# Kernel tuning notes

Hardware: AMD Instinct MI355X
Metric: run time of the kernel (lower is better)

Reference implementation:

```python
import jax, jax.numpy as jnp
import numpy as np

D_MODEL = 1024
EXPAND = 2
D_INNER = D_MODEL * EXPAND  # 2048
D_CONV = 4
B, T = 4, 4096
LN_EPS = 1e-5


def setup_inputs() -> dict:
    key = jax.random.key(0)
    ks = jax.random.split(key, 6)
    x = jax.random.normal(ks[0], (B, T, D_MODEL), dtype=jnp.float32)
    gamma = jnp.ones((D_MODEL,), jnp.float32)
    beta = jnp.zeros((D_MODEL,), jnp.float32)
    # in_proj: Linear(d_model -> 2*d_inner, bias=False); torch weight [out,in]
    W_in = jax.random.normal(ks[1], (2 * D_INNER, D_MODEL), jnp.float32) / np.sqrt(D_MODEL)
    # depthwise conv1d: weight [d_inner, 1, d_conv], bias [d_inner]
    conv_w = jax.random.normal(ks[2], (D_INNER, 1, D_CONV), jnp.float32) / np.sqrt(D_CONV)
    conv_b = jax.random.normal(ks[3], (D_INNER,), jnp.float32) * 0.01
    # out_proj: Linear(d_inner -> d_model, bias=False)
    W_out = jax.random.normal(ks[4], (D_MODEL, D_INNER), jnp.float32) / np.sqrt(D_INNER)
    return {"x": x, "gamma": gamma, "beta": beta, "W_in": W_in,
            "conv_w": conv_w, "conv_b": conv_b, "W_out": W_out}


def _silu(v):
    return v * jax.nn.sigmoid(v)


def reference(x, gamma, beta, W_in, conv_w, conv_b, W_out):
    residual = x
    # LayerNorm
    mu = jnp.mean(x, axis=-1, keepdims=True)
    var = jnp.mean(jnp.square(x - mu), axis=-1, keepdims=True)
    xn = (x - mu) * jax.lax.rsqrt(var + LN_EPS) * gamma + beta
    # in_proj -> split gate
    xz = jnp.einsum('btd,ed->bte', xn, W_in)  # [B,T,2*D_INNER]
    x_part, z = jnp.split(xz, 2, axis=-1)
    # causal depthwise conv: torch pads both sides by d_conv-1 then slices [:T]
    # == left pad (d_conv-1), no right pad
    lhs = jnp.transpose(x_part, (0, 2, 1))  # [B, D_INNER, T]
    x_conv = jax.lax.conv_general_dilated(
        lhs, conv_w, window_strides=(1,), padding=[(D_CONV - 1, 0)],
        feature_group_count=D_INNER,
        dimension_numbers=('NCH', 'OIH', 'NCH')) + conv_b[None, :, None]
    x_conv = jnp.transpose(x_conv, (0, 2, 1))  # [B,T,D_INNER]
    y = _silu(x_conv) * _silu(z)
    out = jnp.einsum('bte,de->btd', y, W_out)
    return residual + out  # dropout=0 (eval) -> identity
```

## Files before the change

kernel.cpp:

```cpp
#include <hip/hip_runtime.h>
#include <hip/hip_bf16.h>

#define D_MODEL 1024
#define D_INNER 2048
#define NTOK    16384
#define TLEN    4096
#define LN_EPS  1e-5f

typedef unsigned short u16;
typedef unsigned short u16x4 __attribute__((ext_vector_type(4)));
typedef unsigned short u16x8 __attribute__((ext_vector_type(8)));
typedef __bf16        bf16x8 __attribute__((ext_vector_type(8)));
typedef float         f32x4  __attribute__((ext_vector_type(4)));

__device__ __forceinline__ float b2f(u16 u) {
    union { float f; unsigned int i; } v; v.i = ((unsigned int)u) << 16; return v.f;
}
__device__ __forceinline__ u16 f2b(float f) {
    union { float f; unsigned int i; } v; v.f = f;
    unsigned int r = v.i + 0x7fffu + ((v.i >> 16) & 1u);
    return (u16)(r >> 16);
}

__device__ __forceinline__ void gld_lds16(const u16* g, u16* l) {
    __builtin_amdgcn_global_load_lds(
        (const __attribute__((address_space(1))) void*)g,
        (__attribute__((address_space(3))) void*)l, 16, 0, 0);
}

__device__ __forceinline__ void ln_body(
    int row, int tid,
    const float* __restrict__ x, const float* __restrict__ gamma,
    const float* __restrict__ beta, u16* __restrict__ xn)
{
    const float* xr = x + (size_t)row * D_MODEL;
    const int c0 = tid * 4;

    f32x4 xv = *(const f32x4*)(xr + c0);
    float s = 0.f, s2 = 0.f;
#pragma unroll
    for (int i = 0; i < 4; i++) { s += xv[i]; s2 += xv[i] * xv[i]; }

#pragma unroll
    for (int off = 32; off > 0; off >>= 1) {
        s  += __shfl_down(s,  off);
        s2 += __shfl_down(s2, off);
    }
    __shared__ float red[8];
    const int wave = tid >> 6, lane = tid & 63;
    if (lane == 0) { red[wave] = s; red[4 + wave] = s2; }
    __syncthreads();
    const float ts  = red[0] + red[1] + red[2] + red[3];
    const float ts2 = red[4] + red[5] + red[6] + red[7];
    const float mu  = ts * (1.0f / D_MODEL);
    const float var = ts2 * (1.0f / D_MODEL) - mu * mu;
    const float inv = rsqrtf(var + LN_EPS);

    f32x4 gv = *(const f32x4*)(gamma + c0);
    f32x4 bv = *(const f32x4*)(beta + c0);
    u16x4 out;
#pragma unroll
    for (int i = 0; i < 4; i++)
        out[i] = f2b((xv[i] - mu) * inv * gv[i] + bv[i]);
    *(u16x4*)(xn + (size_t)row * D_MODEL + c0) = out;
}

__global__ __launch_bounds__(256) void prep_kernel(
    const float* __restrict__ x, const float* __restrict__ gamma,
    const float* __restrict__ beta, u16* __restrict__ xn,
    const float* __restrict__ W_in, u16* __restrict__ wbin,
    const float* __restrict__ W_out, u16* __restrict__ wbout,
    const float* __restrict__ conv_w, float* __restrict__ wt,
    int lnRows)
{
    const int b   = blockIdx.x;
    const int tid = threadIdx.x;

    if (b < lnRows) {
        ln_body(b, tid, x, gamma, beta, xn);
        return;
    }
    int rb = b - lnRows;
    if (rb < 4096) {
        const int o = (rb * 256 + tid) * 4;
        f32x4 v = *(const f32x4*)(W_in + o);
        u16x4 w;
#pragma unroll
        for (int j = 0; j < 4; j++) w[j] = f2b(v[j]);
        *(u16x4*)(wbin + o) = w;
        return;
    }
    rb -= 4096;
    if (rb < 2048) {
        const int o = (rb * 256 + tid) * 4;
        f32x4 v = *(const f32x4*)(W_out + o);
        u16x4 w;
#pragma unroll
        for (int j = 0; j < 4; j++) w[j] = f2b(v[j]);
        *(u16x4*)(wbout + o) = w;
        return;
    }
    rb -= 2048;
    const int i = rb * 256 + tid;
    const int ch = i >> 2, j = i & 3;
    wt[j * D_INNER + ch] = conv_w[i];
}

__global__ __launch_bounds__(256) void ln_kernel(
    const float* __restrict__ x, const float* __restrict__ gamma,
    const float* __restrict__ beta, u16* __restrict__ xn)
{
    ln_body(blockIdx.x, threadIdx.x, x, gamma, beta, xn);
}

#define BAR()      __builtin_amdgcn_s_barrier()
#define WAIT_VM8() asm volatile("s_waitcnt vmcnt(8)" ::: "memory")
#define WAIT_VM4() asm volatile("s_waitcnt vmcnt(4)" ::: "memory")
#define WAIT_VM0() asm volatile("s_waitcnt vmcnt(0)" ::: "memory")

#define STAGE_A(ldsb, s0, s1, kt) do { \
    gld_lds16(Ag + (size_t)(s0) * K + (kt) + goff, &(ldsb)[(s0) * 64]); \
    gld_lds16(Ag + (size_t)(s1) * K + (kt) + goff, &(ldsb)[(s1) * 64]); \
} while (0)
#define STAGE_B(ldsb, s0, s1, kt) do { \
    gld_lds16(Bg + (size_t)(s0) * K + (kt) + goff, &(ldsb)[(s0) * 64]); \
    gld_lds16(Bg + (size_t)(s1) * K + (kt) + goff, &(ldsb)[(s1) * 64]); \
} while (0)

#define RD_A(base, roff) do { \
    _Pragma("unroll") for (int m_ = 0; m_ < 4; m_++) { \
        const u16* p_ = (base) + (arow0 + (roff) + m_ * 16) * 64; \
        aF[m_][0] = __builtin_bit_cast(bf16x8, *(const u16x8*)(p_ + cx0)); \
        aF[m_][1] = __builtin_bit_cast(bf16x8, *(const u16x8*)(p_ + cx1)); \
    } } while (0)
#define RD_B(base, dst, roff) do { \
    _Pragma("unroll") for (int n_ = 0; n_ < 2; n_++) { \
        const u16* p_ = (base) + (brow0 + (roff) + n_ * 16) * 64; \
        dst[n_][0] = __builtin_bit_cast(bf16x8, *(const u16x8*)(p_ + cx0)); \
        dst[n_][1] = __builtin_bit_cast(bf16x8, *(const u16x8*)(p_ + cx1)); \
    } } while (0)

#define MMA_Q(m0, n0, BB) do { \
    __builtin_amdgcn_s_setprio(1); \
    _Pragma("unroll") for (int m_ = 0; m_ < 4; m_++) \
    _Pragma("unroll") for (int n_ = 0; n_ < 2; n_++) \
    _Pragma("unroll") for (int k_ = 0; k_ < 2; k_++) \
        acc[(m0) + m_][(n0) + n_] = __builtin_amdgcn_mfma_f32_16x16x32_bf16( \
            aF[m_][k_], BB[n_][k_], acc[(m0) + m_][(n0) + n_], 0, 0, 0); \
    __builtin_amdgcn_s_setprio(0); \
} while (0)

template<bool OUT_F32>
__global__ __launch_bounds__(512, 2) void gemm256(
    const u16* __restrict__ A, const u16* __restrict__ Bt,
    void* __restrict__ Cv, const float* __restrict__ Res,
    int M, int N, int K)
{
    __shared__ u16 As[2][256 * 64];
    __shared__ u16 Bs[2][256 * 64];

    const int tid  = threadIdx.x;
    const int wave = tid >> 6;
    const int lane = tid & 63;
    const int wm = wave >> 2, wn = wave & 3;
    const int lane15 = lane & 15, quad = lane >> 4;

    const int gx   = gridDim.x;
    const int nwg  = gx * gridDim.y;
    const int flat = blockIdx.y * gx + blockIdx.x;
    const int q8   = nwg >> 3;
    const int swz  = (flat & 7) * q8 + (flat >> 3);
    const int bm = swz % gx, bn = swz / gx;

    const u16* Ag = A  + (size_t)bm * 256 * K;
    const u16* Bg = Bt + (size_t)bn * 256 * K;

    const int lrow = lane >> 3;
    const int lcol = ((lane & 7) ^ lrow) * 8;
    const size_t goff = (size_t)lrow * K + lcol;

    const int aEv0 = wave * 8,      aEv1 = 128 + wave * 8;
    const int aOd0 = 64 + wave * 8, aOd1 = 192 + wave * 8;
    const int bEv0 = (wave >> 2) * 64 + (wave & 3) * 8, bEv1 = 128 + bEv0;
    const int bOd0 = bEv0 + 32,     bOd1 = bEv1 + 32;

    const int arow0 = wm * 128 + lane15;
    const int brow0 = wn * 64  + lane15;
    const int sw8   = lane15 & 7;
    const int cx0   = ((quad ^ sw8) << 3);
    const int cx1   = cx0 ^ 32;

    f32x4  acc[8][4] = {};
    bf16x8 aF[4][2], bX[2][2], bY[2][2];

    const int NT = K >> 6;
    const int NI = NT >> 1;

    STAGE_A(As[0], aEv0, aEv1, 0);
    STAGE_B(Bs[0], bEv0, bEv1, 0);
    STAGE_A(As[0], aOd0, aOd1, 0);
    STAGE_B(Bs[0], bOd0, bOd1, 0);
    STAGE_A(As[1], aEv0, aEv1, 64);
    STAGE_B(Bs[1], bEv0, bEv1, 64);
    STAGE_A(As[1], aOd0, aOd1, 64);
    STAGE_B(Bs[1], bOd0, bOd1, 64);
    WAIT_VM0();
    BAR();
    RD_A(As[0], 0);
    RD_B(Bs[0], bX, 0);

    for (int i = 0; i < NI; i++) {
        const bool more = (i + 1 < NI);
#pragma unroll
        for (int h = 0; h < 2; h++) {
            u16* as  = As[h];
            u16* bs  = Bs[h];
            const u16* asn = As[h ^ 1];
            const u16* bsn = Bs[h ^ 1];
            const int ktS  = i * 128 + 128 + h * 64;
            const bool gN  = (h == 0) || more;
            const bool gS  = more;
            const bool lastT = (h == 1) && !more;

            if (lastT) WAIT_VM0(); else WAIT_VM8();
            BAR();
            RD_B(bs, bY, 32);
            MMA_Q(0, 0, bX);

            BAR();
            MMA_Q(0, 2, bY);
            RD_A(as, 64);

            if (!lastT) WAIT_VM4();
            BAR();
            MMA_Q(4, 0, bX);
            if (gN) RD_B(bsn, bX, 0);
            if (gS) { STAGE_A(as, aEv0, aEv1, ktS); STAGE_B(bs, bEv0, bEv1, ktS); }

            BAR();
            MMA_Q(4, 2, bY);
            if (gN) RD_A(asn, 0);
            if (gS) { STAGE_A(as, aOd0, aOd1, ktS); STAGE_B(bs, bOd0, bOd1, ktS); }
        }
    }

    const int m0 = bm * 256 + wm * 128 + quad * 4;
    const int n0 = bn * 256 + wn * 64 + lane15;
#pragma unroll
    for (int mf = 0; mf < 8; mf++) {
#pragma unroll
        for (int nf = 0; nf < 4; nf++) {
#pragma unroll
            for (int i = 0; i < 4; i++) {
                const int r  = m0 + mf * 16 + i;
                const int cc = n0 + nf * 16;
                const size_t idx = (size_t)r * N + cc;
                float v = acc[mf][nf][i];
                if (OUT_F32) {
                    ((float*)Cv)[idx] = v + Res[idx];
                } else {
                    ((u16*)Cv)[idx] = f2b(v);
                }
            }
        }
    }
}

__global__ __launch_bounds__(256) void conv_gate8(
    const u16* __restrict__ xz, const float* __restrict__ wt,
    const float* __restrict__ conv_b, u16* __restrict__ y)
{
    const int tid  = threadIdx.x;
    const int row0 = blockIdx.x * 8;
    const int c    = tid * 8;
    const int t0   = row0 & (TLEN - 1);

    float w[4][8];
#pragma unroll
    for (int j = 0; j < 4; j++) {
        f32x4 a = *(const f32x4*)(wt + j * D_INNER + c);
        f32x4 b = *(const f32x4*)(wt + j * D_INNER + c + 4);
#pragma unroll
        for (int u = 0; u < 4; u++) { w[j][u] = a[u]; w[j][4 + u] = b[u]; }
    }
    float bias[8];
    {
        f32x4 a = *(const f32x4*)(conv_b + c);
        f32x4 b = *(const f32x4*)(conv_b + c + 4);
#pragma unroll
        for (int u = 0; u < 4; u++) { bias[u] = a[u]; bias[4 + u] = b[u]; }
    }

    u16x8 xv[11];
    if (t0 != 0) {
#pragma unroll
        for (int k = 0; k < 3; k++)
            xv[k] = *(const u16x8*)(xz + (size_t)(row0 - 3 + k) * 4096 + c);
    } else {
#pragma unroll
        for (int k = 0; k < 3; k++) xv[k] = (u16x8)0;
    }
#pragma unroll
    for (int k = 3; k < 11; k++)
        xv[k] = *(const u16x8*)(xz + (size_t)(row0 - 3 + k) * 4096 + c);

#pragma unroll
    for (int i = 0; i < 8; i++) {
        float acc[8];
#pragma unroll
        for (int u = 0; u < 8; u++) acc[u] = bias[u];
#pragma unroll
        for (int j = 0; j < 4; j++)
#pragma unroll
            for (int u = 0; u < 8; u++)
                acc[u] += b2f(xv[i + j][u]) * w[j][u];

        u16x8 zv = *(const u16x8*)(xz + (size_t)(row0 + i) * 4096 + 2048 + c);
        u16x8 out;
#pragma unroll
        for (int u = 0; u < 8; u++) {
            const float a = acc[u];
            const float z = b2f(zv[u]);
            const float sa = a / (1.0f + __expf(-a));
            const float sz = z / (1.0f + __expf(-z));
            out[u] = f2b(sa * sz);
        }
        *(u16x8*)(y + (size_t)(row0 + i) * (size_t)D_INNER + c) = out;
    }
}

extern "C" void kernel_launch(void* const* d_in, const int* in_sizes, int n_in,
                              void* d_out, int out_size, void* d_ws, size_t ws_size,
                              hipStream_t stream)
{
    const float* x      = (const float*)d_in[0];
    const float* gamma  = (const float*)d_in[1];
    const float* beta   = (const float*)d_in[2];
    const float* W_in   = (const float*)d_in[3];
    const float* conv_w = (const float*)d_in[4];
    const float* conv_b = (const float*)d_in[5];
    const float* W_out  = (const float*)d_in[6];
    float* out = (float*)d_out;

    const int nWin  = 4096 * 1024;
    const int nWout = 1024 * 2048;
    const int nWc   = D_INNER * 4;

    u16*   wbin  = (u16*)d_ws;
    u16*   wbout = wbin + nWin;
    float* wt    = (float*)(wbout + nWout);
    u16*   base  = (u16*)(wt + nWc);

    const size_t wbytes = (size_t)(nWin + nWout) * sizeof(u16) + nWc * sizeof(float);
    const size_t perRow = (size_t)(D_MODEL + 4096 + D_INNER) * sizeof(u16);
    int NC = 4;
    if (ws_size >= wbytes + (size_t)NTOK * perRow)          NC = 1;
    else if (ws_size >= wbytes + (size_t)(NTOK/2) * perRow) NC = 2;
    const int RC = NTOK / NC;

    u16* xn = base;
    u16* xz = xn + (size_t)RC * D_MODEL;
    u16* y  = xz + (size_t)RC * 4096;

    const int lnRows = (NC == 1) ? NTOK : 0;
    prep_kernel<<<lnRows + 4096 + 2048 + 32, 256, 0, stream>>>(
        x, gamma, beta, xn, W_in, wbin, W_out, wbout, conv_w, wt, lnRows);

    for (int c = 0; c < NC; c++) {
        const float* xc   = x   + (size_t)c * RC * D_MODEL;
        float*       outc = out + (size_t)c * RC * D_MODEL;

        if (NC > 1)
            ln_kernel<<<RC, 256, 0, stream>>>(xc, gamma, beta, xn);

        dim3 g1(RC / 256, (2 * D_INNER) / 256);
        gemm256<false><<<g1, 512, 0, stream>>>(xn, wbin, xz, nullptr,
                                               RC, 2 * D_INNER, D_MODEL);

        conv_gate8<<<RC / 8, 256, 0, stream>>>(xz, wt, conv_b, y);

        dim3 g2(RC / 256, D_MODEL / 256);
        gemm256<true><<<g2, 512, 0, stream>>>(y, wbout, outc, xc,
                                              RC, D_MODEL, D_INNER);
    }
}
```

Measured before the change: 389.6 us.

## Restructure GEMM to 4 waves with 128x128 per-wave tiles

The 256x256 GEMM block goes from 8 waves (512 threads, 2 blocks/CU) to 4 waves (256 threads, 1 block/CU). Each wave now computes a 128x128 sub-tile with 8x8 accumulators, and staging loads are redistributed so each wave issues four loads per stage. The MFMA setprio hints are removed and the vmcnt waits are adjusted for the larger per-wave load count. This raises per-wave reuse of LDS fragments and cuts LDS read traffic, but it lowers occupancy and greatly increases register pressure (256 accumulator floats per lane), which risks spills and less latency hiding.

```diff
diff --git a/kernel.cpp b/kernel.cpp
--- a/kernel.cpp
+++ b/kernel.cpp
@@ -113,45 +113,35 @@
     ln_body(blockIdx.x, threadIdx.x, x, gamma, beta, xn);
 }
 
-#define BAR()      __builtin_amdgcn_s_barrier()
-#define WAIT_VM8() asm volatile("s_waitcnt vmcnt(8)" ::: "memory")
-#define WAIT_VM4() asm volatile("s_waitcnt vmcnt(4)" ::: "memory")
-#define WAIT_VM0() asm volatile("s_waitcnt vmcnt(0)" ::: "memory")
-
-#define STAGE_A(ldsb, s0, s1, kt) do { \
-    gld_lds16(Ag + (size_t)(s0) * K + (kt) + goff, &(ldsb)[(s0) * 64]); \
-    gld_lds16(Ag + (size_t)(s1) * K + (kt) + goff, &(ldsb)[(s1) * 64]); \
+#define BAR()       __builtin_amdgcn_s_barrier()
+#define WAIT_VM16() asm volatile("s_waitcnt vmcnt(16)" ::: "memory")
+#define WAIT_VM8()  asm volatile("s_waitcnt vmcnt(8)" ::: "memory")
+#define WAIT_VM0()  asm volatile("s_waitcnt vmcnt(0)" ::: "memory")
+
+#define STAGE4(gp, ldsb, c0, kt) do { \
+    gld_lds16((gp) + (size_t)(c0)         * K + (kt) + goff, &(ldsb)[(c0)         * 64]); \
+    gld_lds16((gp) + (size_t)((c0) +   8) * K + (kt) + goff, &(ldsb)[((c0) +   8) * 64]); \
+    gld_lds16((gp) + (size_t)((c0) + 128) * K + (kt) + goff, &(ldsb)[((c0) + 128) * 64]); \
+    gld_lds16((gp) + (size_t)((c0) + 136) * K + (kt) + goff, &(ldsb)[((c0) + 136) * 64]); \
 } while (0)
-#define STAGE_B(ldsb, s0, s1, kt) do { \
-    gld_lds16(Bg + (size_t)(s0) * K + (kt) + goff, &(ldsb)[(s0) * 64]); \
-    gld_lds16(Bg + (size_t)(s1) * K + (kt) + goff, &(ldsb)[(s1) * 64]); \
-} while (0)
-
-#define RD_A(base, roff) do { \
-    _Pragma("unroll") for (int m_ = 0; m_ < 4; m_++) { \
-        const u16* p_ = (base) + (arow0 + (roff) + m_ * 16) * 64; \
-        aF[m_][0] = __builtin_bit_cast(bf16x8, *(const u16x8*)(p_ + cx0)); \
-        aF[m_][1] = __builtin_bit_cast(bf16x8, *(const u16x8*)(p_ + cx1)); \
+
+#define RD4(dst, base, row0, roff) do { \
+    _Pragma("unroll") for (int t_ = 0; t_ < 4; t_++) { \
+        const u16* p_ = (base) + ((row0) + (roff) + t_ * 16) * 64; \
+        dst[t_][0] = __builtin_bit_cast(bf16x8, *(const u16x8*)(p_ + cx0)); \
+        dst[t_][1] = __builtin_bit_cast(bf16x8, *(const u16x8*)(p_ + cx1)); \
     } } while (0)
-#define RD_B(base, dst, roff) do { \
-    _Pragma("unroll") for (int n_ = 0; n_ < 2; n_++) { \
-        const u16* p_ = (base) + (brow0 + (roff) + n_ * 16) * 64; \
-        dst[n_][0] = __builtin_bit_cast(bf16x8, *(const u16x8*)(p_ + cx0)); \
-        dst[n_][1] = __builtin_bit_cast(bf16x8, *(const u16x8*)(p_ + cx1)); \
-    } } while (0)
-
-#define MMA_Q(m0, n0, BB) do { \
-    __builtin_amdgcn_s_setprio(1); \
+
+#define MMA_Q(m0, n0, AA, BB) do { \
     _Pragma("unroll") for (int m_ = 0; m_ < 4; m_++) \
-    _Pragma("unroll") for (int n_ = 0; n_ < 2; n_++) \
+    _Pragma("unroll") for (int n_ = 0; n_ < 4; n_++) \
     _Pragma("unroll") for (int k_ = 0; k_ < 2; k_++) \
         acc[(m0) + m_][(n0) + n_] = __builtin_amdgcn_mfma_f32_16x16x32_bf16( \
-            aF[m_][k_], BB[n_][k_], acc[(m0) + m_][(n0) + n_], 0, 0, 0); \
-    __builtin_amdgcn_s_setprio(0); \
+            AA[m_][k_], BB[n_][k_], acc[(m0) + m_][(n0) + n_], 0, 0, 0); \
 } while (0)
 
 template<bool OUT_F32>
-__global__ __launch_bounds__(512, 2) void gemm256(
+__global__ __launch_bounds__(256, 1) void gemm256(
     const u16* __restrict__ A, const u16* __restrict__ Bt,
     void* __restrict__ Cv, const float* __restrict__ Res,
     int M, int N, int K)
@@ -162,7 +152,7 @@
     const int tid  = threadIdx.x;
     const int wave = tid >> 6;
     const int lane = tid & 63;
-    const int wm = wave >> 2, wn = wave & 3;
+    const int wm2 = wave >> 1, wn2 = wave & 1;
     const int lane15 = lane & 15, quad = lane >> 4;
 
     const int gx   = gridDim.x;
@@ -179,42 +169,36 @@
     const int lcol = ((lane & 7) ^ lrow) * 8;
     const size_t goff = (size_t)lrow * K + lcol;
 
-    const int aEv0 = wave * 8,      aEv1 = 128 + wave * 8;
-    const int aOd0 = 64 + wave * 8, aOd1 = 192 + wave * 8;
-    const int bEv0 = (wave >> 2) * 64 + (wave & 3) * 8, bEv1 = 128 + bEv0;
-    const int bOd0 = bEv0 + 32,     bOd1 = bEv1 + 32;
-
-    const int arow0 = wm * 128 + lane15;
-    const int brow0 = wn * 64  + lane15;
+    const int sEv = wave * 16;
+    const int sOd = 64 + wave * 16;
+
+    const int arow0 = wm2 * 128 + lane15;
+    const int brow0 = wn2 * 128 + lane15;
     const int sw8   = lane15 & 7;
     const int cx0   = ((quad ^ sw8) << 3);
     const int cx1   = cx0 ^ 32;
 
-    f32x4  acc[8][4] = {};
-    bf16x8 aF[4][2], bX[2][2], bY[2][2];
+    f32x4  acc[8][8] = {};
+    bf16x8 a0[4][2], a1[4][2], b0[4][2], b1[4][2];
 
     const int NT = K >> 6;
     const int NI = NT >> 1;
 
-    STAGE_A(As[0], aEv0, aEv1, 0);
-    STAGE_B(Bs[0], bEv0, bEv1, 0);
-    STAGE_A(As[0], aOd0, aOd1, 0);
-    STAGE_B(Bs[0], bOd0, bOd1, 0);
-    STAGE_A(As[1], aEv0, aEv1, 64);
-    STAGE_B(Bs[1], bEv0, bEv1, 64);
-    STAGE_A(As[1], aOd0, aOd1, 64);
-    STAGE_B(Bs[1], bOd0, bOd1, 64);
-    WAIT_VM0();
+    STAGE4(Ag, As[0], sEv, 0);  STAGE4(Bg, Bs[0], sEv, 0);
+    STAGE4(Ag, As[0], sOd, 0);  STAGE4(Bg, Bs[0], sOd, 0);
+    STAGE4(Ag, As[1], sEv, 64); STAGE4(Bg, Bs[1], sEv, 64);
+    STAGE4(Ag, As[1], sOd, 64); STAGE4(Bg, Bs[1], sOd, 64);
+    WAIT_VM16();
     BAR();
-    RD_A(As[0], 0);
-    RD_B(Bs[0], bX, 0);
+    RD4(a0, As[0], arow0, 0);
+    RD4(b0, Bs[0], brow0, 0);
 
     for (int i = 0; i < NI; i++) {
         const bool more = (i + 1 < NI);
 #pragma unroll
         for (int h = 0; h < 2; h++) {
-            u16* as  = As[h];
-            u16* bs  = Bs[h];
+            u16* as = As[h];
+            u16* bs = Bs[h];
             const u16* asn = As[h ^ 1];
             const u16* bsn = Bs[h ^ 1];
             const int ktS  = i * 128 + 128 + h * 64;
@@ -222,34 +206,33 @@
             const bool gS  = more;
             const bool lastT = (h == 1) && !more;
 
-            if (lastT) WAIT_VM0(); else WAIT_VM8();
+            if (lastT) WAIT_VM0(); else WAIT_VM16();
             BAR();
-            RD_B(bs, bY, 32);
-            MMA_Q(0, 0, bX);
+            RD4(b1, bs, brow0, 64);
+            MMA_Q(0, 0, a0, b0);
 
             BAR();
-            MMA_Q(0, 2, bY);
-            RD_A(as, 64);
-
-            if (!lastT) WAIT_VM4();
+            MMA_Q(0, 4, a0, b1);
+            RD4(a1, as, arow0, 64);
+
+            if (!lastT) WAIT_VM8();
             BAR();
-            MMA_Q(4, 0, bX);
-            if (gN) RD_B(bsn, bX, 0);
-            if (gS) { STAGE_A(as, aEv0, aEv1, ktS); STAGE_B(bs, bEv0, bEv1, ktS); }
+            MMA_Q(4, 0, a1, b0);
+            if (gS) { STAGE4(Ag, as, sEv, ktS); STAGE4(Bg, bs, sEv, ktS); }
 
             BAR();
-            MMA_Q(4, 2, bY);
-            if (gN) RD_A(asn, 0);
-            if (gS) { STAGE_A(as, aOd0, aOd1, ktS); STAGE_B(bs, bOd0, bOd1, ktS); }
+            MMA_Q(4, 4, a1, b1);
+            if (gN) { RD4(b0, bsn, brow0, 0); RD4(a0, asn, arow0, 0); }
+            if (gS) { STAGE4(Ag, as, sOd, ktS); STAGE4(Bg, bs, sOd, ktS); }
         }
     }
 
-    const int m0 = bm * 256 + wm * 128 + quad * 4;
-    const int n0 = bn * 256 + wn * 64 + lane15;
+    const int m0 = bm * 256 + wm2 * 128 + quad * 4;
+    const int n0 = bn * 256 + wn2 * 128 + lane15;
 #pragma unroll
     for (int mf = 0; mf < 8; mf++) {
 #pragma unroll
-        for (int nf = 0; nf < 4; nf++) {
+        for (int nf = 0; nf < 8; nf++) {
 #pragma unroll
             for (int i = 0; i < 4; i++) {
                 const int r  = m0 + mf * 16 + i;
@@ -374,13 +357,13 @@
             ln_kernel<<<RC, 256, 0, stream>>>(xc, gamma, beta, xn);
 
         dim3 g1(RC / 256, (2 * D_INNER) / 256);
-        gemm256<false><<<g1, 512, 0, stream>>>(xn, wbin, xz, nullptr,
+        gemm256<false><<<g1, 256, 0, stream>>>(xn, wbin, xz, nullptr,
                                                RC, 2 * D_INNER, D_MODEL);
 
         conv_gate8<<<RC / 8, 256, 0, stream>>>(xz, wt, conv_b, y);
 
         dim3 g2(RC / 256, D_MODEL / 256);
-        gemm256<true><<<g2, 512, 0, stream>>>(y, wbout, outc, xc,
+        gemm256<true><<<g2, 256, 0, stream>>>(y, wbout, outc, xc,
                                               RC, D_MODEL, D_INNER);
     }
 }
```

Measured after the change: 508.1 us. 1.3x slower.
